# Kernel tuning notes

Hardware: AMD Instinct MI355X
Metric: run time of the kernel (lower is better)

## Reference

```python
import jax, jax.numpy as jnp
import numpy as np

B, S, V, E, H, T = 128, 512, 50000, 300, 256, 9


def setup_inputs() -> dict:
    key = jax.random.key(0)
    ks = jax.random.split(key, 20)
    def n(k, shape, s=0.1):
        return (jax.random.normal(k, shape, jnp.float32) * s).astype(jnp.float32)
    return {
        "x": jax.random.randint(ks[0], (B, S), 1, V),           # nonzero -> mask all True
        "tags": jax.random.randint(ks[1], (B, S), 0, T),
        "emb": n(ks[2], (V, E)),
        "Wih_l0f": n(ks[3], (4 * H, E)), "Whh_l0f": n(ks[4], (4 * H, H)), "b_l0f": n(ks[5], (4 * H,)),
        "Wih_l0b": n(ks[6], (4 * H, E)), "Whh_l0b": n(ks[7], (4 * H, H)), "b_l0b": n(ks[8], (4 * H,)),
        "Wih_l1f": n(ks[9], (4 * H, 2 * H)), "Whh_l1f": n(ks[10], (4 * H, H)), "b_l1f": n(ks[11], (4 * H,)),
        "Wih_l1b": n(ks[12], (4 * H, 2 * H)), "Whh_l1b": n(ks[13], (4 * H, H)), "b_l1b": n(ks[14], (4 * H,)),
        "fc_w": n(ks[15], (T, 2 * H)), "fc_b": n(ks[16], (T,)),
        "crf_start": n(ks[17], (T,)), "crf_end": n(ks[18], (T,)), "crf_trans": n(ks[19], (T, T)),
    }


def _lstm_dir(x, Wih, Whh, b, reverse):
    # x: [B,S,D] -> hidden states [B,S,H]; PyTorch gate order i,f,g,o
    Bx, Hh = x.shape[0], Whh.shape[1]
    xs = jnp.swapaxes(x, 0, 1)  # [S,B,D]
    if reverse:
        xs = xs[::-1]
    xW = xs @ Wih.T + b  # precompute input projection [S,B,4H]
    def step(carry, g_in):
        h, c = carry
        g = g_in + h @ Whh.T
        i, f, gg, o = jnp.split(g, 4, axis=-1)
        c = jax.nn.sigmoid(f) * c + jax.nn.sigmoid(i) * jnp.tanh(gg)
        h = jax.nn.sigmoid(o) * jnp.tanh(c)
        return (h, c), h
    h0 = jnp.zeros((Bx, Hh), x.dtype)
    _, hs = jax.lax.scan(step, (h0, h0), xW)
    if reverse:
        hs = hs[::-1]
    return jnp.swapaxes(hs, 0, 1)


def _crf_nll(emissions, tags, mask, start, end, trans):
    # torchcrf: llh = numerator(score of gold path) - log-partition; return mean NLL
    mf = mask.astype(emissions.dtype)
    em_tag = jnp.take_along_axis(emissions, tags[..., None], axis=2)[..., 0]  # [B,S]
    num = start[tags[:, 0]] + em_tag[:, 0]
    trans_sc = trans[tags[:, :-1], tags[:, 1:]]  # [B,S-1]
    num = num + jnp.sum((trans_sc + em_tag[:, 1:]) * mf[:, 1:], axis=1)
    last = jnp.sum(mask.astype(jnp.int32), axis=1) - 1
    last_tags = jnp.take_along_axis(tags, last[:, None], axis=1)[:, 0]
    num = num + end[last_tags]
    # forward algorithm
    alpha = start[None, :] + emissions[:, 0]  # [B,T]
    em_t = jnp.swapaxes(emissions[:, 1:], 0, 1)  # [S-1,B,T]
    m_t = jnp.swapaxes(mask[:, 1:], 0, 1)        # [S-1,B]
    def step(alpha, inp):
        em, m = inp
        nxt = jax.scipy.special.logsumexp(alpha[:, :, None] + trans[None] + em[:, None, :], axis=1)
        return jnp.where(m[:, None], nxt, alpha), None
    alpha, _ = jax.lax.scan(step, alpha, (em_t, m_t))
    denom = jax.scipy.special.logsumexp(alpha + end[None, :], axis=1)
    return jnp.mean(denom - num)


def reference(x, tags, emb, Wih_l0f, Whh_l0f, b_l0f, Wih_l0b, Whh_l0b, b_l0b,
              Wih_l1f, Whh_l1f, b_l1f, Wih_l1b, Whh_l1b, b_l1b,
              fc_w, fc_b, crf_start, crf_end, crf_trans):
    mask = (x != 0)
    e = emb[x]  # [B,S,E]
    l0 = jnp.concatenate([_lstm_dir(e, Wih_l0f, Whh_l0f, b_l0f, False),
                          _lstm_dir(e, Wih_l0b, Whh_l0b, b_l0b, True)], axis=-1)
    l1 = jnp.concatenate([_lstm_dir(l0, Wih_l1f, Whh_l1f, b_l1f, False),
                          _lstm_dir(l0, Wih_l1b, Whh_l1b, b_l1b, True)], axis=-1)
    emissions = l1 @ fc_w.T + fc_b  # [B,S,T] (dropout = identity in eval)
    return _crf_nll(emissions, tags, mask, crf_start, crf_end, crf_trans)
```

## Files before the change

### kernel.cpp

```cpp
#include <hip/hip_runtime.h>
#include <cstdint>
#include <cstddef>

#define BATCH   128
#define SEQ     512
#define TOKENS  (BATCH * SEQ)
#define EMB_D   300
#define KA0     320
#define HID     256
#define G4H     1024
#define KA1     512
#define NTAGS   9
#define CHUNK   128
#define CTOK    (BATCH * CHUNK)

typedef _Float16 f16;
typedef _Float16 f16x2 __attribute__((ext_vector_type(2)));
typedef _Float16 f16x8 __attribute__((ext_vector_type(8)));
typedef float    f32x4 __attribute__((ext_vector_type(4)));

static constexpr size_t XW_BYTES   = (size_t)2 * CTOK * G4H * 2;
static constexpr size_t H_BYTES    = (size_t)TOKENS * KA1 * 2;
static constexpr size_t POOL_BYTES = H_BYTES;
static constexpr size_t EM_BYTES   = (size_t)TOKENS * 16 * 4;
static constexpr size_t WHH_BYTES  = (size_t)4 * G4H * HID * 2;
static constexpr size_t WIH0_BYTES = (size_t)2 * G4H * KA0 * 2;
static constexpr size_t WIH1_BYTES = (size_t)2 * G4H * KA1 * 2;
static constexpr size_t FCW_BYTES  = (size_t)128 * KA1 * 2;
static constexpr size_t FCB_BYTES  = 512;
static constexpr size_t STH_BYTES  = (size_t)2 * BATCH * HID * 2;
static constexpr size_t STC_BYTES  = (size_t)2 * BATCH * HID * 4;
static constexpr size_t NLL_BYTES  = 512;

static constexpr size_t OFF_XW   = 0;
static constexpr size_t OFF_H0   = OFF_XW   + XW_BYTES;
static constexpr size_t OFF_POOL = OFF_H0   + H_BYTES;
static constexpr size_t OFF_EM   = OFF_POOL + POOL_BYTES;
static constexpr size_t OFF_WHH  = OFF_EM   + EM_BYTES;
static constexpr size_t OFF_WIH0 = OFF_WHH  + WHH_BYTES;
static constexpr size_t OFF_WIH1 = OFF_WIH0 + WIH0_BYTES;
static constexpr size_t OFF_FCW  = OFF_WIH1 + WIH1_BYTES;
static constexpr size_t OFF_FCB  = OFF_FCW  + FCW_BYTES;
static constexpr size_t OFF_STH  = OFF_FCB  + FCB_BYTES;
static constexpr size_t OFF_STC  = OFF_STH  + STH_BYTES;
static constexpr size_t OFF_NLL  = OFF_STC  + STC_BYTES;
static constexpr size_t WS_NEEDED = OFF_NLL + NLL_BYTES;

__device__ inline float fdot2(uint32_t a, uint32_t b, float c) {
#if __has_builtin(__builtin_amdgcn_fdot2)
  return __builtin_amdgcn_fdot2(__builtin_bit_cast(f16x2, a),
                                __builtin_bit_cast(f16x2, b), c, false);
#else
  f16x2 ha = __builtin_bit_cast(f16x2, a), hb = __builtin_bit_cast(f16x2, b);
  return c + (float)ha.x * (float)hb.x + (float)ha.y * (float)hb.y;
#endif
}

__device__ inline int swz(int r, int q) { return q ^ ((r & 3) ^ ((r >> 2) & 3)); }

__global__ void prep_kernel(
    const float* whh_l0f, const float* whh_l0b, const float* whh_l1f, const float* whh_l1b,
    const float* wih_l0f, const float* wih_l0b,
    const float* wih_l1f, const float* wih_l1b,
    const float* fc_w, const float* fc_b,
    f16* whh16, f16* wih0_16, f16* wih1_16, f16* fcw16, float* fcb32)
{
  int id = blockIdx.x * 256 + threadIdx.x;
  if (id < 1048576) {
    int which = id >> 18; int off = id & 262143;
    const float* s = which == 0 ? whh_l0f : which == 1 ? whh_l0b
                   : which == 2 ? whh_l1f : whh_l1b;
    whh16[id] = (f16)s[off];
    return;
  }
  id -= 1048576;
  if (id < 655360) {
    int dir = id / 327680; int rem = id - dir * 327680;
    int r = rem / KA0; int k = rem - r * KA0;
    const float* s = dir ? wih_l0b : wih_l0f;
    wih0_16[id] = (f16)(k < EMB_D ? s[r * EMB_D + k] : 0.f);
    return;
  }
  id -= 655360;
  if (id < 1048576) {
    const float* s = (id < 524288) ? wih_l1f : wih_l1b;
    wih1_16[id] = (f16)s[id & 524287];
    return;
  }
  id -= 1048576;
  if (id < 65536) {
    int r = id >> 9;
    fcw16[id] = (f16)(r < NTAGS ? fc_w[id] : 0.f);
    return;
  }
  id -= 65536;
  if (id < 128) fcb32[id] = id < NTAGS ? fc_b[id] : 0.f;
}

__global__ void embed_kernel(const int* __restrict__ x, const float* __restrict__ emb,
                             f16* __restrict__ e16)
{
  int id = blockIdx.x * 256 + threadIdx.x;
  if (id >= TOKENS * KA0) return;
  int row = id / KA0, k = id - row * KA0;
  float v = 0.f;
  if (k < EMB_D) v = emb[(size_t)x[row] * EMB_D + k];
  e16[id] = (f16)v;
}

__global__ __launch_bounds__(256, 3) void gemm_kernel(
    const f16* __restrict__ A, int lda, int aGrpStride,
    const f16* __restrict__ B0, const f16* __restrict__ B1, int ldb,
    const float* __restrict__ bias0, const float* __restrict__ bias1,
    f16* outH, float* outF, int ldc, size_t outZStride,
    int kChunks, int nLimit, int cbF, int cbB)
{
  __shared__ __align__(16) f16 As[128 * 32];
  __shared__ __align__(16) f16 Bs[128 * 32];
  const int z = blockIdx.z;
  const f16* B = z ? B1 : B0;
  const float* bias = z ? bias1 : bias0;
  const int cb = z ? cbB : cbF;
  const int m0 = blockIdx.x * 128, n0 = blockIdx.y * 128;
  const int aBase = (m0 >> 7) * aGrpStride + cb;
  const int tid = threadIdx.x;
  const int w = tid >> 6, lane = tid & 63;
  const int mw = (w & 1) * 64, nw = (w >> 1) * 64;
  const int fr = lane & 15, fq = lane >> 4;

  f32x4 acc[4][4];
#pragma unroll
  for (int i = 0; i < 4; ++i)
#pragma unroll
    for (int j = 0; j < 4; ++j) acc[i][j] = (f32x4)(0.f);

  const int c0 = tid, c1 = tid + 256;
  const int r0 = c0 >> 2, q0 = c0 & 3, r1c = c1 >> 2, q1 = c1 & 3;

  for (int kc = 0; kc < kChunks; ++kc) {
    const int k0 = kc * 32;
    uint4 a0v = *(const uint4*)(A + (size_t)(aBase + r0)  * lda + k0 + q0 * 8);
    uint4 a1v = *(const uint4*)(A + (size_t)(aBase + r1c) * lda + k0 + q1 * 8);
    uint4 b0v = *(const uint4*)(B + (size_t)(n0 + r0)  * ldb + k0 + q0 * 8);
    uint4 b1v = *(const uint4*)(B + (size_t)(n0 + r1c) * ldb + k0 + q1 * 8);
    __syncthreads();
    *(uint4*)(As + r0  * 32 + swz(r0,  q0) * 8) = a0v;
    *(uint4*)(As + r1c * 32 + swz(r1c, q1) * 8) = a1v;
    *(uint4*)(Bs + r0  * 32 + swz(r0,  q0) * 8) = b0v;
    *(uint4*)(Bs + r1c * 32 + swz(r1c, q1) * 8) = b1v;
    __syncthreads();
    f16x8 af[4], bf[4];
#pragma unroll
    for (int i = 0; i < 4; ++i) {
      int rr = mw + i * 16 + fr;
      af[i] = *(const f16x8*)(As + rr * 32 + swz(rr, fq) * 8);
    }
#pragma unroll
    for (int j = 0; j < 4; ++j) {
      int rr = nw + j * 16 + fr;
      bf[j] = *(const f16x8*)(Bs + rr * 32 + swz(rr, fq) * 8);
    }
#pragma unroll
    for (int i = 0; i < 4; ++i)
#pragma unroll
      for (int j = 0; j < 4; ++j)
        acc[i][j] = __builtin_amdgcn_mfma_f32_16x16x32_f16(af[i], bf[j], acc[i][j], 0, 0, 0);
  }
  f16* oH = outH ? outH + (size_t)z * outZStride : nullptr;
  float* oF = outF;
#pragma unroll
  for (int j = 0; j < 4; ++j) {
    int n = n0 + nw + j * 16 + fr;
    if (n >= nLimit) continue;
    float bs = bias ? bias[n] : 0.f;
#pragma unroll
    for (int i = 0; i < 4; ++i) {
#pragma unroll
      for (int r = 0; r < 4; ++r) {
        int m = m0 + mw + i * 16 + fq * 4 + r;
        float v = acc[i][j][r] + bs;
        if (oH) oH[(size_t)m * ldc + n] = (f16)v;
        else    oF[(size_t)m * ldc + n] = v;
      }
    }
  }
}

__global__ __launch_bounds__(512, 2) void rec_kernel(
    const uint32_t* __restrict__ xw,
    const uint32_t* __restrict__ whh_f, const uint32_t* __restrict__ whh_b,
    f16* __restrict__ hout,
    f16* __restrict__ stateH, float* __restrict__ stateC, int r)
{
  __shared__ __align__(16) uint4 wlds[16 * 512];
  __shared__ float gates[1024];
  __shared__ __align__(16) f16 hbuf[2][256];
  const int tau = threadIdx.x;
  const int bid = blockIdx.x;
  const int dir = bid >> 7;
  const int b   = bid & 127;
  const int chunk = dir ? (3 - r) : r;
  const int tBase = chunk * CHUNK;
  const uint32_t* whh = dir ? whh_b : whh_f;
  const uint32_t* xwp = xw + (size_t)(dir * 128 + b) * CHUNK * 512;

  const int row0 = 2 * tau, row1 = 2 * tau + 1;
  uint4 wa4[24], wb4[24];
  {
    const uint4* p0 = (const uint4*)(whh + row0 * 128);
    const uint4* p1 = (const uint4*)(whh + row1 * 128);
#pragma unroll
    for (int i = 0; i < 24; ++i) { wa4[i] = p0[i]; wb4[i] = p1[i]; }
#pragma unroll
    for (int c = 0; c < 16; ++c) {
      uint4 v;
      v.x = whh[row0 * 128 + 96 + 2 * c]; v.y = whh[row0 * 128 + 97 + 2 * c];
      v.z = whh[row1 * 128 + 96 + 2 * c]; v.w = whh[row1 * 128 + 97 + 2 * c];
      wlds[c * 512 + tau] = v;
    }
  }
  float cst = 0.f;
  if (tau < 256) {
    f16 hi = (f16)0.f;
    if (r) { hi = stateH[(dir * 128 + b) * 256 + tau]; cst = stateC[(dir * 128 + b) * 256 + tau]; }
    hbuf[0][tau] = hi;
  }
  __syncthreads();

  int lr0 = dir ? (CHUNK - 1) : 0;
  uint32_t xw_cur = xwp[lr0 * 512 + tau];

  for (int s = 0; s < CHUNK; ++s) {
    const int lrow = dir ? (CHUNK - 1 - s) : s;
    const size_t token = (size_t)b * 512 + tBase + lrow;
    const int cur = s & 1, nxt = cur ^ 1;
    uint32_t xw_nextv = 0;
    if (s < CHUNK - 1) {
      int lrn = dir ? (CHUNK - 2 - s) : (s + 1);
      xw_nextv = xwp[lrn * 512 + tau];
    }
    f16x2 xh = __builtin_bit_cast(f16x2, xw_cur);
    float a0 = (float)xh.x, a1 = (float)xh.y;
    const uint4* hb4 = (const uint4*)hbuf[cur];
#pragma unroll
    for (int i = 0; i < 24; ++i) {
      uint4 hv = hb4[i];
      a0 = fdot2(wa4[i].x, hv.x, a0);
      a0 = fdot2(wa4[i].y, hv.y, a0);
      a0 = fdot2(wa4[i].z, hv.z, a0);
      a0 = fdot2(wa4[i].w, hv.w, a0);
      a1 = fdot2(wb4[i].x, hv.x, a1);
      a1 = fdot2(wb4[i].y, hv.y, a1);
      a1 = fdot2(wb4[i].z, hv.z, a1);
      a1 = fdot2(wb4[i].w, hv.w, a1);
    }
#pragma unroll
    for (int c2 = 0; c2 < 8; ++c2) {
      uint4 hv = hb4[24 + c2];
      uint4 w0 = wlds[(2 * c2) * 512 + tau];
      uint4 w1 = wlds[(2 * c2 + 1) * 512 + tau];
      a0 = fdot2(w0.x, hv.x, a0); a0 = fdot2(w0.y, hv.y, a0);
      a1 = fdot2(w0.z, hv.x, a1); a1 = fdot2(w0.w, hv.y, a1);
      a0 = fdot2(w1.x, hv.z, a0); a0 = fdot2(w1.y, hv.w, a0);
      a1 = fdot2(w1.z, hv.z, a1); a1 = fdot2(w1.w, hv.w, a1);
    }
    gates[row0] = a0; gates[row1] = a1;
    __syncthreads();
    if (tau < 256) {
      float gi = gates[tau], gf = gates[256 + tau], gg = gates[512 + tau], go = gates[768 + tau];
      float si = 1.f / (1.f + __expf(-gi));
      float sf = 1.f / (1.f + __expf(-gf));
      float so = 1.f / (1.f + __expf(-go));
      float e2 = __expf(2.f * gg); float tg = 1.f - 2.f / (e2 + 1.f);
      cst = sf * cst + si * tg;
      e2 = __expf(2.f * cst); float tc = 1.f - 2.f / (e2 + 1.f);
      float h = so * tc;
      f16 hh = (f16)h;
      hbuf[nxt][tau] = hh;
      hout[token * 512 + dir * 256 + tau] = hh;
    }
    __syncthreads();
    xw_cur = xw_nextv;
  }
  if (tau < 256) {
    stateH[(dir * 128 + b) * 256 + tau] = hbuf[0][tau];
    stateC[(dir * 128 + b) * 256 + tau] = cst;
  }
}

__global__ void crf_kernel(const float* __restrict__ em, const int* __restrict__ tags,
                           const float* __restrict__ start, const float* __restrict__ endv,
                           const float* __restrict__ trans, float* __restrict__ nll)
{
  const int b = blockIdx.x;
  const int lane = threadIdx.x;
  const float* emb_ = em + (size_t)b * SEQ * 16;
  const int* tg = tags + b * SEQ;

  float numacc = 0.f;
  for (int t = lane; t < SEQ; t += 64) {
    int ct = tg[t];
    numacc += emb_[t * 16 + ct];
    if (t > 0) numacc += trans[tg[t - 1] * NTAGS + ct];
  }
#pragma unroll
  for (int s = 32; s; s >>= 1) numacc += __shfl_xor(numacc, s);

  int jj = lane < NTAGS ? lane : 0;
  float tr[NTAGS];
#pragma unroll
  for (int i = 0; i < NTAGS; ++i) tr[i] = trans[i * NTAGS + jj];
  float alpha = (lane < NTAGS) ? (start[lane] + emb_[lane]) : -1e30f;
  for (int t = 1; t < SEQ; ++t) {
    float va[NTAGS];
#pragma unroll
    for (int i = 0; i < NTAGS; ++i) va[i] = __shfl(alpha, i) + tr[i];
    float mx = va[0];
#pragma unroll
    for (int i = 1; i < NTAGS; ++i) mx = fmaxf(mx, va[i]);
    float s = 0.f;
#pragma unroll
    for (int i = 0; i < NTAGS; ++i) s += __expf(va[i] - mx);
    float na = mx + __logf(s) + emb_[t * 16 + jj];
    alpha = (lane < NTAGS) ? na : -1e30f;
  }
  float v = (lane < NTAGS) ? alpha + endv[lane] : -1e30f;
  float mx = v;
#pragma unroll
  for (int s2 = 32; s2; s2 >>= 1) mx = fmaxf(mx, __shfl_xor(mx, s2));
  float se = __expf(v - mx);
#pragma unroll
  for (int s2 = 32; s2; s2 >>= 1) se += __shfl_xor(se, s2);
  float denom = mx + __logf(se);
  if (lane == 0) {
    float num = numacc + start[tg[0]] + endv[tg[SEQ - 1]];
    nll[b] = denom - num;
  }
}

__global__ void reduce_kernel(const float* __restrict__ nll, float* __restrict__ out) {
  int lane = threadIdx.x;
  float v = nll[lane] + nll[lane + 64];
#pragma unroll
  for (int s = 32; s; s >>= 1) v += __shfl_xor(v, s);
  if (lane == 0) out[0] = v * (1.f / 128.f);
}

extern "C" void kernel_launch(void* const* d_in, const int* in_sizes, int n_in,
                              void* d_out, int out_size, void* d_ws, size_t ws_size,
                              hipStream_t stream)
{
  const int*   x        = (const int*)d_in[0];
  const int*   tags     = (const int*)d_in[1];
  const float* emb      = (const float*)d_in[2];
  const float* wih_l0f  = (const float*)d_in[3];
  const float* whh_l0f  = (const float*)d_in[4];
  const float* b_l0f    = (const float*)d_in[5];
  const float* wih_l0b  = (const float*)d_in[6];
  const float* whh_l0b  = (const float*)d_in[7];
  const float* b_l0b    = (const float*)d_in[8];
  const float* wih_l1f  = (const float*)d_in[9];
  const float* whh_l1f  = (const float*)d_in[10];
  const float* b_l1f    = (const float*)d_in[11];
  const float* wih_l1b  = (const float*)d_in[12];
  const float* whh_l1b  = (const float*)d_in[13];
  const float* b_l1b    = (const float*)d_in[14];
  const float* fc_w     = (const float*)d_in[15];
  const float* fc_b     = (const float*)d_in[16];
  const float* crf_start= (const float*)d_in[17];
  const float* crf_end  = (const float*)d_in[18];
  const float* crf_trans= (const float*)d_in[19];

  char* ws = (char*)d_ws;
  f16*   xw16   = (f16*)(ws + OFF_XW);
  f16*   h0     = (f16*)(ws + OFF_H0);
  f16*   e16    = (f16*)(ws + OFF_POOL);
  f16*   h1     = (f16*)(ws + OFF_POOL);
  float* em32   = (float*)(ws + OFF_EM);
  f16*   whh16  = (f16*)(ws + OFF_WHH);
  f16*   wih016 = (f16*)(ws + OFF_WIH0);
  f16*   wih116 = (f16*)(ws + OFF_WIH1);
  f16*   fcw16  = (f16*)(ws + OFF_FCW);
  float* fcb32  = (float*)(ws + OFF_FCB);
  f16*   stH    = (f16*)(ws + OFF_STH);
  float* stC    = (float*)(ws + OFF_STC);
  float* nllbuf = (float*)(ws + OFF_NLL);
  const uint32_t* xw32  = (const uint32_t*)xw16;
  const uint32_t* whh32 = (const uint32_t*)whh16;

  prep_kernel<<<11009, 256, 0, stream>>>(whh_l0f, whh_l0b, whh_l1f, whh_l1b,
                                         wih_l0f, wih_l0b, wih_l1f, wih_l1b,
                                         fc_w, fc_b, whh16, wih016, wih116, fcw16, fcb32);
  embed_kernel<<<(TOKENS * KA0) / 256, 256, 0, stream>>>(x, emb, e16);

  const size_t zstr = (size_t)CTOK * G4H;
  dim3 gch(CTOK / 128, G4H / 128, 2);

  for (int r = 0; r < 4; ++r) {
    gemm_kernel<<<gch, 256, 0, stream>>>(e16, KA0, SEQ,
                                         wih016, wih016 + (size_t)G4H * KA0, KA0,
                                         b_l0f, b_l0b, xw16, nullptr, G4H, zstr,
                                         KA0 / 32, G4H, r * CHUNK, (3 - r) * CHUNK);
    rec_kernel<<<256, 512, 0, stream>>>(xw32, whh32, whh32 + (size_t)G4H * 128,
                                        h0, stH, stC, r);
  }

  for (int r = 0; r < 4; ++r) {
    gemm_kernel<<<gch, 256, 0, stream>>>(h0, KA1, SEQ,
                                         wih116, wih116 + (size_t)G4H * KA1, KA1,
                                         b_l1f, b_l1b, xw16, nullptr, G4H, zstr,
                                         KA1 / 32, G4H, r * CHUNK, (3 - r) * CHUNK);
    rec_kernel<<<256, 512, 0, stream>>>(xw32, whh32 + (size_t)2 * G4H * 128,
                                        whh32 + (size_t)3 * G4H * 128,
                                        h1, stH, stC, r);
  }

  dim3 gfc(TOKENS / 128, 1, 1);
  gemm_kernel<<<gfc, 256, 0, stream>>>(h1, KA1, 128,
                                       fcw16, nullptr, KA1, fcb32, nullptr,
                                       nullptr, em32, 16, 0, KA1 / 32, 16, 0, 0);

  crf_kernel<<<BATCH, 64, 0, stream>>>(em32, tags, crf_start, crf_end, crf_trans, nllbuf);
  reduce_kernel<<<1, 64, 0, stream>>>(nllbuf, (float*)d_out);
}
```

Measured before the change: 2.568 ms.

## Use one thread per gate row in LSTM recurrence with 1024-thread blocks

The recurrent kernel moves from 512 threads, each computing two gate rows, to 1024 threads, each computing one row. Each thread keeps 23 uint4 of its Whh row in registers and stages the remaining 9 uint4 in LDS, and the input projection is read as one f16 per thread. The goal is to halve the serial dot-product chain per timestep and put more waves in flight to hide latency. The cost is a larger LDS footprint (9×1024 uint4), twice as many threads hitting the per-step barriers, and higher register pressure per CU, which may limit occupancy.

Measured after the change: 2.997 ms. 16.7% more time.

```diff
diff --git a/kernel.cpp b/kernel.cpp
--- a/kernel.cpp
+++ b/kernel.cpp
@@ -13,6 +13,9 @@
 #define NTAGS   9
 #define CHUNK   128
 #define CTOK    (BATCH * CHUNK)
+
+#define WREG    23
+#define WLDS    9
 
 typedef _Float16 f16;
 typedef _Float16 f16x2 __attribute__((ext_vector_type(2)));
@@ -44,7 +47,6 @@
 static constexpr size_t OFF_STH  = OFF_FCB  + FCB_BYTES;
 static constexpr size_t OFF_STC  = OFF_STH  + STH_BYTES;
 static constexpr size_t OFF_NLL  = OFF_STC  + STC_BYTES;
-static constexpr size_t WS_NEEDED = OFF_NLL + NLL_BYTES;
 
 __device__ inline float fdot2(uint32_t a, uint32_t b, float c) {
 #if __has_builtin(__builtin_amdgcn_fdot2)
@@ -186,13 +188,13 @@
   }
 }
 
-__global__ __launch_bounds__(512, 2) void rec_kernel(
-    const uint32_t* __restrict__ xw,
+__global__ __launch_bounds__(1024, 4) void rec_kernel(
+    const f16* __restrict__ xw,
     const uint32_t* __restrict__ whh_f, const uint32_t* __restrict__ whh_b,
     f16* __restrict__ hout,
     f16* __restrict__ stateH, float* __restrict__ stateC, int r)
 {
-  __shared__ __align__(16) uint4 wlds[16 * 512];
+  __shared__ __align__(16) uint4 wlds[WLDS * 1024];
   __shared__ float gates[1024];
   __shared__ __align__(16) f16 hbuf[2][256];
   const int tau = threadIdx.x;
@@ -202,22 +204,15 @@
   const int chunk = dir ? (3 - r) : r;
   const int tBase = chunk * CHUNK;
   const uint32_t* whh = dir ? whh_b : whh_f;
-  const uint32_t* xwp = xw + (size_t)(dir * 128 + b) * CHUNK * 512;
-
-  const int row0 = 2 * tau, row1 = 2 * tau + 1;
-  uint4 wa4[24], wb4[24];
+  const f16* xwp = xw + (size_t)(dir * 128 + b) * CHUNK * 1024;
+
+  uint4 wa4[WREG];
   {
-    const uint4* p0 = (const uint4*)(whh + row0 * 128);
-    const uint4* p1 = (const uint4*)(whh + row1 * 128);
-#pragma unroll
-    for (int i = 0; i < 24; ++i) { wa4[i] = p0[i]; wb4[i] = p1[i]; }
-#pragma unroll
-    for (int c = 0; c < 16; ++c) {
-      uint4 v;
-      v.x = whh[row0 * 128 + 96 + 2 * c]; v.y = whh[row0 * 128 + 97 + 2 * c];
-      v.z = whh[row1 * 128 + 96 + 2 * c]; v.w = whh[row1 * 128 + 97 + 2 * c];
-      wlds[c * 512 + tau] = v;
-    }
+    const uint4* p0 = (const uint4*)(whh + tau * 128);
+#pragma unroll
+    for (int i = 0; i < WREG; ++i) wa4[i] = p0[i];
+#pragma unroll
+    for (int c = 0; c < WLDS; ++c) wlds[c * 1024 + tau] = p0[WREG + c];
   }
   float cst = 0.f;
   if (tau < 256) {
@@ -228,43 +223,37 @@
   __syncthreads();
 
   int lr0 = dir ? (CHUNK - 1) : 0;
-  uint32_t xw_cur = xwp[lr0 * 512 + tau];
+  f16 xw_cur = xwp[lr0 * 1024 + tau];
 
   for (int s = 0; s < CHUNK; ++s) {
     const int lrow = dir ? (CHUNK - 1 - s) : s;
     const size_t token = (size_t)b * 512 + tBase + lrow;
     const int cur = s & 1, nxt = cur ^ 1;
-    uint32_t xw_nextv = 0;
+    f16 xw_nextv = (f16)0.f;
     if (s < CHUNK - 1) {
       int lrn = dir ? (CHUNK - 2 - s) : (s + 1);
-      xw_nextv = xwp[lrn * 512 + tau];
-    }
-    f16x2 xh = __builtin_bit_cast(f16x2, xw_cur);
-    float a0 = (float)xh.x, a1 = (float)xh.y;
+      xw_nextv = xwp[lrn * 1024 + tau];
+    }
+    float a0 = (float)xw_cur;
     const uint4* hb4 = (const uint4*)hbuf[cur];
 #pragma unroll
-    for (int i = 0; i < 24; ++i) {
+    for (int c = 0; c < WLDS; ++c) {
+      uint4 hv = hb4[WREG + c];
+      uint4 wv = wlds[c * 1024 + tau];
+      a0 = fdot2(wv.x, hv.x, a0);
+      a0 = fdot2(wv.y, hv.y, a0);
+      a0 = fdot2(wv.z, hv.z, a0);
+      a0 = fdot2(wv.w, hv.w, a0);
+    }
+#pragma unroll
+    for (int i = 0; i < WREG; ++i) {
       uint4 hv = hb4[i];
       a0 = fdot2(wa4[i].x, hv.x, a0);
       a0 = fdot2(wa4[i].y, hv.y, a0);
       a0 = fdot2(wa4[i].z, hv.z, a0);
       a0 = fdot2(wa4[i].w, hv.w, a0);
-      a1 = fdot2(wb4[i].x, hv.x, a1);
-      a1 = fdot2(wb4[i].y, hv.y, a1);
-      a1 = fdot2(wb4[i].z, hv.z, a1);
-      a1 = fdot2(wb4[i].w, hv.w, a1);
-    }
-#pragma unroll
-    for (int c2 = 0; c2 < 8; ++c2) {
-      uint4 hv = hb4[24 + c2];
-      uint4 w0 = wlds[(2 * c2) * 512 + tau];
-      uint4 w1 = wlds[(2 * c2 + 1) * 512 + tau];
-      a0 = fdot2(w0.x, hv.x, a0); a0 = fdot2(w0.y, hv.y, a0);
-      a1 = fdot2(w0.z, hv.x, a1); a1 = fdot2(w0.w, hv.y, a1);
-      a0 = fdot2(w1.x, hv.z, a0); a0 = fdot2(w1.y, hv.w, a0);
-      a1 = fdot2(w1.z, hv.z, a1); a1 = fdot2(w1.w, hv.w, a1);
-    }
-    gates[row0] = a0; gates[row1] = a1;
+    }
+    gates[tau] = a0;
     __syncthreads();
     if (tau < 256) {
       float gi = gates[tau], gf = gates[256 + tau], gg = gates[512 + tau], go = gates[768 + tau];
@@ -385,7 +374,6 @@
   f16*   stH    = (f16*)(ws + OFF_STH);
   float* stC    = (float*)(ws + OFF_STC);
   float* nllbuf = (float*)(ws + OFF_NLL);
-  const uint32_t* xw32  = (const uint32_t*)xw16;
   const uint32_t* whh32 = (const uint32_t*)whh16;
 
   prep_kernel<<<11009, 256, 0, stream>>>(whh_l0f, whh_l0b, whh_l1f, whh_l1b,
@@ -401,8 +389,8 @@
                                          wih016, wih016 + (size_t)G4H * KA0, KA0,
                                          b_l0f, b_l0b, xw16, nullptr, G4H, zstr,
                                          KA0 / 32, G4H, r * CHUNK, (3 - r) * CHUNK);
-    rec_kernel<<<256, 512, 0, stream>>>(xw32, whh32, whh32 + (size_t)G4H * 128,
-                                        h0, stH, stC, r);
+    rec_kernel<<<256, 1024, 0, stream>>>(xw16, whh32, whh32 + (size_t)G4H * 128,
+                                         h0, stH, stC, r);
   }
 
   for (int r = 0; r < 4; ++r) {
@@ -410,9 +398,9 @@
                                          wih116, wih116 + (size_t)G4H * KA1, KA1,
                                          b_l1f, b_l1b, xw16, nullptr, G4H, zstr,
                                          KA1 / 32, G4H, r * CHUNK, (3 - r) * CHUNK);
-    rec_kernel<<<256, 512, 0, stream>>>(xw32, whh32 + (size_t)2 * G4H * 128,
-                                        whh32 + (size_t)3 * G4H * 128,
-                                        h1, stH, stC, r);
+    rec_kernel<<<256, 1024, 0, stream>>>(xw16, whh32 + (size_t)2 * G4H * 128,
+                                         whh32 + (size_t)3 * G4H * 128,
+                                         h1, stH, stC, r);
   }
 
   dim3 gfc(TOKENS / 128, 1, 1);
```
